# Performance work log

Hardware: AMD Instinct MI355X
Metric: run time of the kernel (lower is better)

The kernel has to match this reference:

```python
import jax, jax.numpy as jnp
import numpy as np

B, E, H, NF, NO, L = 1024, 256, 4, 16384, 49152, 192
DH = E // H
NEG = -1e9  # effectively -inf for masked-out padded keys


def _positions(batch, n, offset_counts=None):
    # batch is sorted; within-segment index = i - segment_start[batch[i]]
    counts = jax.ops.segment_sum(jnp.ones((n,), jnp.int32), batch, num_segments=B)
    start = jnp.cumsum(counts) - counts
    pos = jnp.arange(n, dtype=jnp.int32) - start[batch]
    if offset_counts is not None:
        pos = pos + offset_counts[batch]
    return pos, counts


def setup_inputs() -> dict:
    key = jax.random.key(0)
    ks = jax.random.split(key, 8)
    scene_feat = jax.random.normal(ks[0], (B, E), jnp.float32)
    face_nodes = jax.random.normal(ks[1], (NF, E), jnp.float32)
    obj_nodes = jax.random.normal(ks[2], (NO, E), jnp.float32)
    face_batch = jnp.sort(jax.random.randint(ks[3], (NF,), 0, B))
    obj_batch = jnp.sort(jax.random.randint(ks[4], (NO,), 0, B))
    s = 1.0 / np.sqrt(E)
    in_proj_w = jax.random.uniform(ks[5], (3 * E, E), jnp.float32, -s, s)
    in_proj_b = jnp.zeros((3 * E,), jnp.float32)
    out_proj_w = jax.random.uniform(ks[6], (E, E), jnp.float32, -s, s)
    out_proj_b = jnp.zeros((E,), jnp.float32)
    ln_gamma = jnp.ones((E,), jnp.float32)
    ln_beta = jnp.zeros((E,), jnp.float32)
    return dict(scene_feat=scene_feat, face_nodes=face_nodes, obj_nodes=obj_nodes,
                face_batch=face_batch, obj_batch=obj_batch,
                in_proj_w=in_proj_w, in_proj_b=in_proj_b,
                out_proj_w=out_proj_w, out_proj_b=out_proj_b,
                ln_gamma=ln_gamma, ln_beta=ln_beta)


def reference(scene_feat, face_nodes, obj_nodes, face_batch, obj_batch,
              in_proj_w, in_proj_b, out_proj_w, out_proj_b, ln_gamma, ln_beta):
    # --- to_dense_batch over concat([face, obj]) : faces first per graph ---
    pos_f, counts_f = _positions(face_batch, NF)
    pos_o, _ = _positions(obj_batch, NO, offset_counts=counts_f)
    all_nodes = jnp.concatenate([face_nodes, obj_nodes], axis=0)   # [N, E]
    all_batch = jnp.concatenate([face_batch, obj_batch], axis=0)   # [N]
    all_pos = jnp.concatenate([pos_f, pos_o], axis=0)              # [N]
    slot = jnp.where(all_pos < L, all_pos, L)                      # overflow -> sentinel col
    dense = jnp.zeros((B, L + 1, E), all_nodes.dtype).at[all_batch, slot].set(all_nodes)[:, :L]
    mask = jnp.zeros((B, L + 1), bool).at[all_batch, slot].set(True)[:, :L]

    # --- single-query multihead cross-attention (torch MHA semantics) ---
    wq, wk, wv = in_proj_w[:E], in_proj_w[E:2 * E], in_proj_w[2 * E:]
    bq, bk, bv = in_proj_b[:E], in_proj_b[E:2 * E], in_proj_b[2 * E:]
    q = (scene_feat @ wq.T + bq).reshape(B, H, DH)                 # [B,H,DH]
    k = (dense @ wk.T + bk).reshape(B, L, H, DH)
    v = (dense @ wv.T + bv).reshape(B, L, H, DH)
    scores = jnp.einsum('bhd,blhd->bhl', q, k) / np.sqrt(DH)        # [B,H,L]
    scores = jnp.where(mask[:, None, :], scores, NEG)
    attn = jax.nn.softmax(scores, axis=-1)                          # [B,H,L]
    ctx = jnp.einsum('bhl,blhd->bhd', attn, v).reshape(B, E)
    attn_out = ctx @ out_proj_w.T + out_proj_b                      # [B,E]

    # --- residual + LayerNorm ---
    x = scene_feat + attn_out
    mu = jnp.mean(x, axis=-1, keepdims=True)
    var = jnp.mean(jnp.square(x - mu), axis=-1, keepdims=True)
    fused = (x - mu) * jax.lax.rsqrt(var + 1e-5) * ln_gamma + ln_beta  # [B,E]

    attn_weights = jnp.mean(attn, axis=1)[:, None, :]               # [B,1,L] head-averaged
    return fused, attn_weights
```

## Files before the change

### kernel.cpp

```cpp
#include <hip/hip_runtime.h>
#include <math.h>

#define B 1024
#define E 256
#define H 4
#define DH 64
#define L 192
#define NF 16384
#define NO 49152
#define BPB 2

__global__ __launch_bounds__(256) void prep_kernel(
    const int* __restrict__ fb, const int* __restrict__ ob,
    int* __restrict__ start_f, int* __restrict__ start_o,
    const float* __restrict__ ipw, const float* __restrict__ opw,
    float* __restrict__ WT)
{
  int blk = blockIdx.x;
  if (blk < 192) {
    int m = blk / 64;
    int r = blk % 64;
    int bx = (r & 7) * 32, by = (r >> 3) * 32;
    const float* src = (m == 0) ? ipw : (m == 1 ? ipw + 2 * E * E : opw);
    float* dst = WT + (size_t)m * E * E;
    __shared__ float tile[32][33];
    int tx = threadIdx.x & 31, ty = threadIdx.x >> 5;
#pragma unroll
    for (int i = 0; i < 32; i += 8)
      tile[ty + i][tx] = src[(size_t)(by + ty + i) * E + bx + tx];
    __syncthreads();
#pragma unroll
    for (int i = 0; i < 32; i += 8)
      dst[(size_t)(bx + ty + i) * E + by + tx] = tile[tx][ty + i];
  } else {
    int b = (blk - 192) * 256 + threadIdx.x;
    if (b > B) return;
    int lo = 0, hi = NF;
    while (lo < hi) { int m = (lo + hi) >> 1; if (fb[m] < b) lo = m + 1; else hi = m; }
    start_f[b] = lo;
    lo = 0; hi = NO;
    while (lo < hi) { int m = (lo + hi) >> 1; if (ob[m] < b) lo = m + 1; else hi = m; }
    start_o[b] = lo;
  }
}

__global__ __launch_bounds__(512, 2) void fused_kernel(
    const float* __restrict__ scene,
    const float* __restrict__ face, const float* __restrict__ obj,
    const float* __restrict__ ipw, const float* __restrict__ ipb,
    const float* __restrict__ WqT, const float* __restrict__ WvT,
    const float* __restrict__ WoT, const float* __restrict__ opb,
    const float* __restrict__ gamma, const float* __restrict__ beta,
    const int* __restrict__ start_f, const int* __restrict__ start_o,
    float* __restrict__ fusedO, float* __restrict__ attnw)
{
  int b0 = blockIdx.x * BPB;
  int t = threadIdx.x, wave = t >> 6, lane = t & 63;

  __shared__ float sc_s[BPB][E];
  __shared__ float q_s[BPB][E];
  __shared__ float YZ_s[BPB][H][E];
  __shared__ float ctx_s[BPB][E];
  __shared__ float s_s[BPB][H][L];
  __shared__ float un_s[4096];
  __shared__ float mw_s[BPB][2][2][2], su_s[BPB][2][2][2], sb_s[BPB][H];
  __shared__ int   info_s[BPB][4];

  sc_s[t >> 8][t & 255] = scene[(size_t)b0 * E + t];
  if (t < BPB) {
    int b = b0 + t;
    int sf0 = start_f[b], cf = start_f[b + 1] - sf0;
    int so0 = start_o[b], co = start_o[b + 1] - so0;
    info_s[t][0] = sf0; info_s[t][1] = so0;
    info_s[t][2] = min(cf, L); info_s[t][3] = min(cf + co, L);
  }
  __syncthreads();

  {
    const float4* W4 = (const float4*)WqT + lane;
    float4 a0 = {0,0,0,0}, a1 = {0,0,0,0};
    int j0 = wave * 32;
#pragma unroll
    for (int jj = 0; jj < 32; ++jj) {
      int j = j0 + jj;
      float4 w = W4[(size_t)j * 64];
      float s0 = sc_s[0][j], s1 = sc_s[1][j];
      a0.x += s0*w.x; a0.y += s0*w.y; a0.z += s0*w.z; a0.w += s0*w.w;
      a1.x += s1*w.x; a1.y += s1*w.y; a1.z += s1*w.z; a1.w += s1*w.w;
    }
    *(float4*)&un_s[((wave * BPB + 0) << 8) + 4 * lane] = a0;
    *(float4*)&un_s[((wave * BPB + 1) << 8) + 4 * lane] = a1;
  }
  __syncthreads();
  {
    int bi = t >> 8, e = t & 255;
    float v = ipb[e];
#pragma unroll
    for (int w = 0; w < 8; ++w) v += un_s[((w * BPB + bi) << 8) + e];
    q_s[bi][e] = v;
  }
  __syncthreads();

  if (wave < BPB) {
#pragma unroll
    for (int h = 0; h < H; ++h) {
      float v = q_s[wave][h * DH + lane] * ipb[E + h * DH + lane];
#pragma unroll
      for (int o = 32; o; o >>= 1) v += __shfl_xor(v, o);
      if (lane == 0) sb_s[wave][h] = v;
    }
  }

  {
    const float* Wk = ipw + (size_t)E * E;
    int h = wave >> 1, d0 = (wave & 1) * 32, wi = wave & 1;
    float4 a0 = {0,0,0,0}, a1 = {0,0,0,0};
#pragma unroll
    for (int dd = 0; dd < 32; ++dd) {
      int d = d0 + dd;
      float4 w = *((const float4*)(Wk + (size_t)(h * DH + d) * E) + lane);
      float q0 = q_s[0][h * DH + d], q1 = q_s[1][h * DH + d];
      a0.x += q0*w.x; a0.y += q0*w.y; a0.z += q0*w.z; a0.w += q0*w.w;
      a1.x += q1*w.x; a1.y += q1*w.y; a1.z += q1*w.z; a1.w += q1*w.w;
    }
    *(float4*)&un_s[wi * 2048 + ((0 * H + h) << 8) + 4 * lane] = a0;
    *(float4*)&un_s[wi * 2048 + ((1 * H + h) << 8) + 4 * lane] = a1;
  }
  __syncthreads();
  for (int i = t; i < BPB * H * E; i += 512)
    ((float*)YZ_s)[i] = un_s[i] + un_s[2048 + i];
  __syncthreads();

  {
    int bb = wave >> 2, hp = (wave >> 1) & 1, rs = wave & 1, h0 = hp * 2;
    int g = lane >> 4, sl = lane & 15;
    int sf0 = info_s[bb][0], so0 = info_s[bb][1];
    int n_f = info_s[bb][2], n = info_s[bb][3];

    float4 y[2][4];
#pragma unroll
    for (int hh = 0; hh < 2; ++hh)
#pragma unroll
      for (int k = 0; k < 4; ++k)
        y[hh][k] = *(const float4*)&YZ_s[bb][h0 + hh][4 * (sl + 16 * k)];
    float sbv[2] = {sb_s[bb][h0], sb_s[bb][h0 + 1]};

    float m[2] = {-3.0e38f, -3.0e38f};
    float u[2] = {0.f, 0.f};
    float4 acc[2][4] = {};

    int s0 = rs * 4 + g;
    float4 x[4] = {};
    if (s0 < n) {
      const float* xr = (s0 < n_f) ? face + (size_t)(sf0 + s0) * E
                                   : obj  + (size_t)(so0 + s0 - n_f) * E;
#pragma unroll
      for (int k = 0; k < 4; ++k) x[k] = ((const float4*)xr)[sl + 16 * k];
    }

    for (int s = s0; s < n; s += 8) {
      float4 xn[4] = {};
      int sn = s + 8;
      if (sn < n) {
        const float* xr = (sn < n_f) ? face + (size_t)(sf0 + sn) * E
                                     : obj  + (size_t)(so0 + sn - n_f) * E;
#pragma unroll
        for (int k = 0; k < 4; ++k) xn[k] = ((const float4*)xr)[sl + 16 * k];
      }

      float p[2];
#pragma unroll
      for (int hh = 0; hh < 2; ++hh) {
        float a = 0.f;
#pragma unroll
        for (int k = 0; k < 4; ++k)
          a += x[k].x * y[hh][k].x + x[k].y * y[hh][k].y +
               x[k].z * y[hh][k].z + x[k].w * y[hh][k].w;
        p[hh] = a;
      }
#pragma unroll
      for (int off = 8; off; off >>= 1) {
        p[0] += __shfl_xor(p[0], off);
        p[1] += __shfl_xor(p[1], off);
      }
      p[0] = (p[0] + sbv[0]) * 0.125f;
      p[1] = (p[1] + sbv[1]) * 0.125f;
      if (sl == 0) {
        s_s[bb][h0][s] = p[0];
        s_s[bb][h0 + 1][s] = p[1];
      }
#pragma unroll
      for (int hh = 0; hh < 2; ++hh) {
        if (p[hh] > m[hh]) {
          float f = __expf(m[hh] - p[hh]);
#pragma unroll
          for (int k = 0; k < 4; ++k) {
            acc[hh][k].x = acc[hh][k].x * f + x[k].x;
            acc[hh][k].y = acc[hh][k].y * f + x[k].y;
            acc[hh][k].z = acc[hh][k].z * f + x[k].z;
            acc[hh][k].w = acc[hh][k].w * f + x[k].w;
          }
          u[hh] = u[hh] * f + 1.f;
          m[hh] = p[hh];
        } else {
          float e = __expf(p[hh] - m[hh]);
#pragma unroll
          for (int k = 0; k < 4; ++k) {
            acc[hh][k].x += e * x[k].x;
            acc[hh][k].y += e * x[k].y;
            acc[hh][k].z += e * x[k].z;
            acc[hh][k].w += e * x[k].w;
          }
          u[hh] += e;
        }
      }
#pragma unroll
      for (int k = 0; k < 4; ++k) x[k] = xn[k];
    }

#pragma unroll
    for (int off = 16; off <= 32; off <<= 1) {
#pragma unroll
      for (int hh = 0; hh < 2; ++hh) {
        float mo = __shfl_xor(m[hh], off);
        float uo = __shfl_xor(u[hh], off);
        float M = fmaxf(m[hh], mo);
        float fs = __expf(m[hh] - M), fo = __expf(mo - M);
        u[hh] = fs * u[hh] + fo * uo;
        m[hh] = M;
#pragma unroll
        for (int k = 0; k < 4; ++k) {
          float ax = __shfl_xor(acc[hh][k].x, off);
          float ay = __shfl_xor(acc[hh][k].y, off);
          float az = __shfl_xor(acc[hh][k].z, off);
          float aw = __shfl_xor(acc[hh][k].w, off);
          acc[hh][k].x = fs * acc[hh][k].x + fo * ax;
          acc[hh][k].y = fs * acc[hh][k].y + fo * ay;
          acc[hh][k].z = fs * acc[hh][k].z + fo * az;
          acc[hh][k].w = fs * acc[hh][k].w + fo * aw;
        }
      }
    }
    if (g == 0) {
#pragma unroll
      for (int hh = 0; hh < 2; ++hh)
#pragma unroll
        for (int k = 0; k < 4; ++k)
          *(float4*)&un_s[((((bb * 2 + hp) * 2 + rs) * 2 + hh) << 8) + 4 * (sl + 16 * k)] = acc[hh][k];
    }
    if (lane == 0) {
      mw_s[bb][hp][rs][0] = m[0]; mw_s[bb][hp][rs][1] = m[1];
      su_s[bb][hp][rs][0] = u[0]; su_s[bb][hp][rs][1] = u[1];
    }
  }
  __syncthreads();

  for (int i = t; i < BPB * H * E; i += 512) {
    int bi = i >> 10, rem = i & 1023, h = rem >> 8, e = rem & 255;
    float z = 0.f;
    if (info_s[bi][3] > 0) {
      int hp = h >> 1, hh = h & 1;
      float ma = mw_s[bi][hp][0][hh], mb = mw_s[bi][hp][1][hh];
      float M = fmaxf(ma, mb);
      float fa = __expf(ma - M), fb = __expf(mb - M);
      float inv = 1.0f / (fa * su_s[bi][hp][0][hh] + fb * su_s[bi][hp][1][hh]);
      z = (fa * un_s[((((bi * 2 + hp) * 2 + 0) * 2 + hh) << 8) + e] +
           fb * un_s[((((bi * 2 + hp) * 2 + 1) * 2 + hh) << 8) + e]) * inv;
    }
    ((float*)YZ_s)[i] = z;
  }
  if (t < BPB * L) {
    int bi = t / L, s = t - bi * L;
    int n = info_s[bi][3];
    float v;
    if (n == 0) v = 1.0f / L;
    else if (s < n) {
      v = 0.f;
#pragma unroll
      for (int h = 0; h < H; ++h) {
        int hp = h >> 1, hh = h & 1;
        float ma = mw_s[bi][hp][0][hh], mb = mw_s[bi][hp][1][hh];
        float M = fmaxf(ma, mb);
        float fa = __expf(ma - M), fb = __expf(mb - M);
        float inv = 1.0f / (fa * su_s[bi][hp][0][hh] + fb * su_s[bi][hp][1][hh]);
        v += __expf(s_s[bi][h][s] - M) * inv;
      }
      v *= 0.25f;
    } else v = 0.f;
    attnw[(size_t)(b0 + bi) * L + s] = v;
  }
  __syncthreads();

  {
    const float4* W4 = (const float4*)WvT + lane;
    int j0 = wave * 32, hoff = (lane >> 4) * E;
    float4 a0 = {0,0,0,0}, a1 = {0,0,0,0};
#pragma unroll
    for (int jj = 0; jj < 32; ++jj) {
      int j = j0 + jj;
      float4 w = W4[(size_t)j * 64];
      float z0 = ((float*)YZ_s[0])[hoff + j];
      float z1 = ((float*)YZ_s[1])[hoff + j];
      a0.x += z0*w.x; a0.y += z0*w.y; a0.z += z0*w.z; a0.w += z0*w.w;
      a1.x += z1*w.x; a1.y += z1*w.y; a1.z += z1*w.z; a1.w += z1*w.w;
    }
    *(float4*)&un_s[((wave * BPB + 0) << 8) + 4 * lane] = a0;
    *(float4*)&un_s[((wave * BPB + 1) << 8) + 4 * lane] = a1;
  }
  __syncthreads();
  {
    int bi = t >> 8, e = t & 255;
    float v = ipb[2 * E + e];
#pragma unroll
    for (int w = 0; w < 8; ++w) v += un_s[((w * BPB + bi) << 8) + e];
    ctx_s[bi][e] = v;
  }
  __syncthreads();

  {
    const float4* W4 = (const float4*)WoT + lane;
    int j0 = wave * 32;
    float4 a0 = {0,0,0,0}, a1 = {0,0,0,0};
#pragma unroll
    for (int jj = 0; jj < 32; ++jj) {
      int j = j0 + jj;
      float4 w = W4[(size_t)j * 64];
      float c0 = ctx_s[0][j], c1 = ctx_s[1][j];
      a0.x += c0*w.x; a0.y += c0*w.y; a0.z += c0*w.z; a0.w += c0*w.w;
      a1.x += c1*w.x; a1.y += c1*w.y; a1.z += c1*w.z; a1.w += c1*w.w;
    }
    *(float4*)&un_s[((wave * BPB + 0) << 8) + 4 * lane] = a0;
    *(float4*)&un_s[((wave * BPB + 1) << 8) + 4 * lane] = a1;
  }
  __syncthreads();
  {
    int bi = t >> 8, e = t & 255;
    float v = opb[e] + sc_s[bi][e];
#pragma unroll
    for (int w = 0; w < 8; ++w) v += un_s[((w * BPB + bi) << 8) + e];
    q_s[bi][e] = v;
  }
  __syncthreads();

  if (wave < BPB) {
    float v0 = q_s[wave][lane], v1 = q_s[wave][lane + 64],
          v2 = q_s[wave][lane + 128], v3 = q_s[wave][lane + 192];
    float s1 = v0 + v1 + v2 + v3;
#pragma unroll
    for (int o = 32; o; o >>= 1) s1 += __shfl_xor(s1, o);
    float mu = s1 * (1.0f / E);
    float d0 = v0 - mu, d1 = v1 - mu, d2 = v2 - mu, d3 = v3 - mu;
    float s2 = d0*d0 + d1*d1 + d2*d2 + d3*d3;
#pragma unroll
    for (int o = 32; o; o >>= 1) s2 += __shfl_xor(s2, o);
    float inv = 1.0f / sqrtf(s2 * (1.0f / E) + 1e-5f);
    size_t base = (size_t)(b0 + wave) * E;
    fusedO[base + lane      ] = d0 * inv * gamma[lane      ] + beta[lane      ];
    fusedO[base + lane +  64] = d1 * inv * gamma[lane +  64] + beta[lane +  64];
    fusedO[base + lane + 128] = d2 * inv * gamma[lane + 128] + beta[lane + 128];
    fusedO[base + lane + 192] = d3 * inv * gamma[lane + 192] + beta[lane + 192];
  }
}

extern "C" void kernel_launch(void* const* d_in, const int* in_sizes, int n_in,
                              void* d_out, int out_size, void* d_ws, size_t ws_size,
                              hipStream_t stream) {
  const float* scene = (const float*)d_in[0];
  const float* face  = (const float*)d_in[1];
  const float* obj   = (const float*)d_in[2];
  const int*   fb    = (const int*)d_in[3];
  const int*   ob    = (const int*)d_in[4];
  const float* ipw   = (const float*)d_in[5];
  const float* ipb   = (const float*)d_in[6];
  const float* opw   = (const float*)d_in[7];
  const float* opb   = (const float*)d_in[8];
  const float* gam   = (const float*)d_in[9];
  const float* bet   = (const float*)d_in[10];

  float* fused = (float*)d_out;
  float* attnw = fused + (size_t)B * E;

  int* start_f = (int*)d_ws;
  int* start_o = start_f + (B + 1);
  float* WT   = (float*)((char*)d_ws + (16 << 10));
  float* WqT = WT;
  float* WvT = WT + (size_t)E * E;
  float* WoT = WT + (size_t)2 * E * E;

  prep_kernel<<<197, 256, 0, stream>>>(fb, ob, start_f, start_o, ipw, opw, WT);
  fused_kernel<<<B / BPB, 512, 0, stream>>>(scene, face, obj, ipw, ipb,
                                            WqT, WvT, WoT, opb, gam, bet,
                                            start_f, start_o, fused, attnw);
}
```

Before: 62.06 us.

## Process four batches per 1024-thread block with per-batch wave groups for GEMVs

Doubles batches per block from two to four and the block size to 1024 threads, halving the grid. The Q, K, V and output projections are remapped so each group of four waves owns one batch and splits the reduction dimension four ways. This drops the old double-batch register accumulators and one reduction pass for the K projection. In exchange each weight matrix is now streamed once per batch instead of once per batch pair, which raises cache traffic. The launch bound of four 1024-thread blocks per CU may also force register pressure or spills.

```diff
diff --git a/kernel.cpp b/kernel.cpp
--- a/kernel.cpp
+++ b/kernel.cpp
@@ -8,7 +8,7 @@
 #define L 192
 #define NF 16384
 #define NO 49152
-#define BPB 2
+#define BPB 4
 
 __global__ __launch_bounds__(256) void prep_kernel(
     const int* __restrict__ fb, const int* __restrict__ ob,
@@ -44,7 +44,7 @@
   }
 }
 
-__global__ __launch_bounds__(512, 2) void fused_kernel(
+__global__ __launch_bounds__(1024, 4) void fused_kernel(
     const float* __restrict__ scene,
     const float* __restrict__ face, const float* __restrict__ obj,
     const float* __restrict__ ipw, const float* __restrict__ ipb,
@@ -56,17 +56,18 @@
 {
   int b0 = blockIdx.x * BPB;
   int t = threadIdx.x, wave = t >> 6, lane = t & 63;
+  int bw = wave >> 2, sub = wave & 3;
 
   __shared__ float sc_s[BPB][E];
   __shared__ float q_s[BPB][E];
   __shared__ float YZ_s[BPB][H][E];
   __shared__ float ctx_s[BPB][E];
   __shared__ float s_s[BPB][H][L];
-  __shared__ float un_s[4096];
+  __shared__ float un_s[8192];
   __shared__ float mw_s[BPB][2][2][2], su_s[BPB][2][2][2], sb_s[BPB][H];
   __shared__ int   info_s[BPB][4];
 
-  sc_s[t >> 8][t & 255] = scene[(size_t)b0 * E + t];
+  if (t < BPB * E) ((float*)sc_s)[t] = scene[(size_t)b0 * E + t];
   if (t < BPB) {
     int b = b0 + t;
     int sf0 = start_f[b], cf = start_f[b + 1] - sf0;
@@ -78,26 +79,23 @@
 
   {
     const float4* W4 = (const float4*)WqT + lane;
-    float4 a0 = {0,0,0,0}, a1 = {0,0,0,0};
-    int j0 = wave * 32;
-#pragma unroll
-    for (int jj = 0; jj < 32; ++jj) {
+    const float* sc = sc_s[bw];
+    float4 a = {0.f, 0.f, 0.f, 0.f};
+    int j0 = sub * 64;
+#pragma unroll 8
+    for (int jj = 0; jj < 64; ++jj) {
       int j = j0 + jj;
       float4 w = W4[(size_t)j * 64];
-      float s0 = sc_s[0][j], s1 = sc_s[1][j];
-      a0.x += s0*w.x; a0.y += s0*w.y; a0.z += s0*w.z; a0.w += s0*w.w;
-      a1.x += s1*w.x; a1.y += s1*w.y; a1.z += s1*w.z; a1.w += s1*w.w;
-    }
-    *(float4*)&un_s[((wave * BPB + 0) << 8) + 4 * lane] = a0;
-    *(float4*)&un_s[((wave * BPB + 1) << 8) + 4 * lane] = a1;
-  }
-  __syncthreads();
-  {
+      float s = sc[j];
+      a.x += s * w.x; a.y += s * w.y; a.z += s * w.z; a.w += s * w.w;
+    }
+    *(float4*)&un_s[((sub * BPB + bw) << 8) + 4 * lane] = a;
+  }
+  __syncthreads();
+  if (t < BPB * E) {
     int bi = t >> 8, e = t & 255;
-    float v = ipb[e];
-#pragma unroll
-    for (int w = 0; w < 8; ++w) v += un_s[((w * BPB + bi) << 8) + e];
-    q_s[bi][e] = v;
+    q_s[bi][e] = un_s[((0 * BPB + bi) << 8) + e] + un_s[((1 * BPB + bi) << 8) + e] +
+                 un_s[((2 * BPB + bi) << 8) + e] + un_s[((3 * BPB + bi) << 8) + e] + ipb[e];
   }
   __syncthreads();
 
@@ -110,25 +108,17 @@
       if (lane == 0) sb_s[wave][h] = v;
     }
   }
-
   {
     const float* Wk = ipw + (size_t)E * E;
-    int h = wave >> 1, d0 = (wave & 1) * 32, wi = wave & 1;
-    float4 a0 = {0,0,0,0}, a1 = {0,0,0,0};
-#pragma unroll
-    for (int dd = 0; dd < 32; ++dd) {
-      int d = d0 + dd;
-      float4 w = *((const float4*)(Wk + (size_t)(h * DH + d) * E) + lane);
-      float q0 = q_s[0][h * DH + d], q1 = q_s[1][h * DH + d];
-      a0.x += q0*w.x; a0.y += q0*w.y; a0.z += q0*w.z; a0.w += q0*w.w;
-      a1.x += q1*w.x; a1.y += q1*w.y; a1.z += q1*w.z; a1.w += q1*w.w;
-    }
-    *(float4*)&un_s[wi * 2048 + ((0 * H + h) << 8) + 4 * lane] = a0;
-    *(float4*)&un_s[wi * 2048 + ((1 * H + h) << 8) + 4 * lane] = a1;
-  }
-  __syncthreads();
-  for (int i = t; i < BPB * H * E; i += 512)
-    ((float*)YZ_s)[i] = un_s[i] + un_s[2048 + i];
+    float4 a = {0.f, 0.f, 0.f, 0.f};
+#pragma unroll 8
+    for (int d = 0; d < DH; ++d) {
+      float qv = q_s[bw][sub * DH + d];
+      float4 w = *((const float4*)(Wk + (size_t)(sub * DH + d) * E) + lane);
+      a.x += qv * w.x; a.y += qv * w.y; a.z += qv * w.z; a.w += qv * w.w;
+    }
+    *(float4*)&YZ_s[bw][sub][4 * lane] = a;
+  }
   __syncthreads();
 
   {
@@ -255,7 +245,7 @@
   }
   __syncthreads();
 
-  for (int i = t; i < BPB * H * E; i += 512) {
+  for (int i = t; i < BPB * H * E; i += 1024) {
     int bi = i >> 10, rem = i & 1023, h = rem >> 8, e = rem & 255;
     float z = 0.f;
     if (info_s[bi][3] > 0) {
@@ -293,52 +283,47 @@
 
   {
     const float4* W4 = (const float4*)WvT + lane;
-    int j0 = wave * 32, hoff = (lane >> 4) * E;
-    float4 a0 = {0,0,0,0}, a1 = {0,0,0,0};
-#pragma unroll
-    for (int jj = 0; jj < 32; ++jj) {
+    const float* zr = YZ_s[bw][lane >> 4];
+    float4 a = {0.f, 0.f, 0.f, 0.f};
+    int j0 = sub * 64;
+#pragma unroll 8
+    for (int jj = 0; jj < 64; ++jj) {
       int j = j0 + jj;
       float4 w = W4[(size_t)j * 64];
-      float z0 = ((float*)YZ_s[0])[hoff + j];
-      float z1 = ((float*)YZ_s[1])[hoff + j];
-      a0.x += z0*w.x; a0.y += z0*w.y; a0.z += z0*w.z; a0.w += z0*w.w;
-      a1.x += z1*w.x; a1.y += z1*w.y; a1.z += z1*w.z; a1.w += z1*w.w;
-    }
-    *(float4*)&un_s[((wave * BPB + 0) << 8) + 4 * lane] = a0;
-    *(float4*)&un_s[((wave * BPB + 1) << 8) + 4 * lane] = a1;
-  }
-  __syncthreads();
-  {
+      float zv = zr[j];
+      a.x += zv * w.x; a.y += zv * w.y; a.z += zv * w.z; a.w += zv * w.w;
+    }
+    *(float4*)&un_s[((sub * BPB + bw) << 8) + 4 * lane] = a;
+  }
+  __syncthreads();
+  if (t < BPB * E) {
     int bi = t >> 8, e = t & 255;
-    float v = ipb[2 * E + e];
-#pragma unroll
-    for (int w = 0; w < 8; ++w) v += un_s[((w * BPB + bi) << 8) + e];
-    ctx_s[bi][e] = v;
+    ctx_s[bi][e] = un_s[((0 * BPB + bi) << 8) + e] + un_s[((1 * BPB + bi) << 8) + e] +
+                   un_s[((2 * BPB + bi) << 8) + e] + un_s[((3 * BPB + bi) << 8) + e] +
+                   ipb[2 * E + e];
   }
   __syncthreads();
 
   {
     const float4* W4 = (const float4*)WoT + lane;
-    int j0 = wave * 32;
-    float4 a0 = {0,0,0,0}, a1 = {0,0,0,0};
-#pragma unroll
-    for (int jj = 0; jj < 32; ++jj) {
+    const float* cr = ctx_s[bw];
+    float4 a = {0.f, 0.f, 0.f, 0.f};
+    int j0 = sub * 64;
+#pragma unroll 8
+    for (int jj = 0; jj < 64; ++jj) {
       int j = j0 + jj;
       float4 w = W4[(size_t)j * 64];
-      float c0 = ctx_s[0][j], c1 = ctx_s[1][j];
-      a0.x += c0*w.x; a0.y += c0*w.y; a0.z += c0*w.z; a0.w += c0*w.w;
-      a1.x += c1*w.x; a1.y += c1*w.y; a1.z += c1*w.z; a1.w += c1*w.w;
-    }
-    *(float4*)&un_s[((wave * BPB + 0) << 8) + 4 * lane] = a0;
-    *(float4*)&un_s[((wave * BPB + 1) << 8) + 4 * lane] = a1;
-  }
-  __syncthreads();
-  {
+      float cv = cr[j];
+      a.x += cv * w.x; a.y += cv * w.y; a.z += cv * w.z; a.w += cv * w.w;
+    }
+    *(float4*)&un_s[((sub * BPB + bw) << 8) + 4 * lane] = a;
+  }
+  __syncthreads();
+  if (t < BPB * E) {
     int bi = t >> 8, e = t & 255;
-    float v = opb[e] + sc_s[bi][e];
-#pragma unroll
-    for (int w = 0; w < 8; ++w) v += un_s[((w * BPB + bi) << 8) + e];
-    q_s[bi][e] = v;
+    q_s[bi][e] = un_s[((0 * BPB + bi) << 8) + e] + un_s[((1 * BPB + bi) << 8) + e] +
+                 un_s[((2 * BPB + bi) << 8) + e] + un_s[((3 * BPB + bi) << 8) + e] +
+                 opb[e] + sc_s[bi][e];
   }
   __syncthreads();
 
@@ -388,7 +373,7 @@
   float* WoT = WT + (size_t)2 * E * E;
 
   prep_kernel<<<197, 256, 0, stream>>>(fb, ob, start_f, start_o, ipw, opw, WT);
-  fused_kernel<<<B / BPB, 512, 0, stream>>>(scene, face, obj, ipw, ipb,
-                                            WqT, WvT, WoT, opb, gam, bet,
-                                            start_f, start_o, fused, attnw);
+  fused_kernel<<<B / BPB, 1024, 0, stream>>>(scene, face, obj, ipw, ipb,
+                                             WqT, WvT, WoT, opb, gam, bet,
+                                             start_f, start_o, fused, attnw);
 }
```

Result: slower. 65.25 us (+5.1%).
